# Kernel optimization log

Hardware: AMD Instinct MI355X
Metric: run time of the kernel (lower is better)

Reference implementation:

```python
import jax, jax.numpy as jnp
import numpy as np

C = 32        # channels per degree
NDEG = 4      # degrees 0..3
NLAYERS = 4   # hidden GSE3Res layers
OUTC = 64     # output fiber degree-0 channels
BATCH = 16
NPOINTS = 128
RBF_D = 16


def _sph(u):
    # real spherical harmonics l=0..3 on unit vectors u [E,3]
    x, y, z = u[:, 0], u[:, 1], u[:, 2]
    Y0 = 0.28209479177 * jnp.ones_like(x)[:, None]
    Y1 = 0.48860251190 * jnp.stack([y, z, x], -1)
    Y2 = jnp.stack([1.09254843059 * x * y, 1.09254843059 * y * z,
                    0.31539156525 * (3.0 * z * z - 1.0), 1.09254843059 * x * z,
                    0.54627421529 * (x * x - y * y)], -1)
    Y3 = jnp.stack([0.59004358992 * y * (3.0 * x * x - y * y), 2.89061144264 * x * y * z,
                    0.45704579946 * y * (5.0 * z * z - 1.0), 0.37317633259 * z * (5.0 * z * z - 3.0),
                    0.45704579946 * x * (5.0 * z * z - 1.0), 1.44530572132 * z * (x * x - y * y),
                    0.59004358992 * x * (x * x - 3.0 * y * y)], -1)
    return [Y0, Y1, Y2, Y3]


def _seg_softmax(logits, seg, n):
    m = jax.ops.segment_max(logits, seg, num_segments=n)
    e = jnp.exp(logits - m[seg])
    s = jax.ops.segment_sum(e, seg, num_segments=n)
    return e / s[seg]


def _forward(x, w1, b1, rW, sW, Wv, Wq, Wk, Wo, Wskip, gw, gb,
             w1o, b1o, roW, WvO, WqO, WkO, WoO, WskipO,
             Whid, bhid, Wout, bout, src, dst, gid):
    N = x.shape[0]
    rel = x[dst] - x[src]                                  # [E,3]
    d = jnp.sqrt((rel * rel).sum(-1) + 1e-12)              # [E]
    Ys = _sph(rel / d[:, None])
    centers = jnp.linspace(0.0, 4.0, RBF_D)
    rbf = jnp.exp(-((d[:, None] - centers) ** 2) / (2.0 * 0.5 ** 2))  # [E,16]
    # input fiber {1:1} is zeros_like(x) in the original -> start from zero features
    h = [jnp.zeros((N, C, 2 * l + 1), x.dtype) for l in range(NDEG)]
    for i in range(NLAYERS):
        rh = jax.nn.relu(rbf @ w1[i] + b1[i])              # [E,32] radial net
        q = h[0][:, :, 0] @ Wq[i]                          # [N,32] invariant query
        k = rh @ Wk[i]                                     # [E,32]
        logit = (q[dst] * k).sum(-1) / (C ** 0.5)
        alpha = _seg_softmax(logit, dst, N)
        h0s = h[0][src][:, :, 0]                           # [E,32]
        new = []
        for l in range(NDEG):
            hs = h[l][src]                                 # [E,C,2l+1]
            R = rh @ rW[i, l]                              # [E,C] same-degree radial gate
            S = rh @ sW[i, l]                              # [E,C] degree0->l path
            v = jnp.einsum('ecm,cd->edm', hs, Wv[i, l]) * R[:, :, None]
            v = v + (S * (h0s + 1.0))[:, :, None] * Ys[l][:, None, :]
            agg = jax.ops.segment_sum(alpha[:, None, None] * v, dst, num_segments=N)
            hn = (jnp.einsum('ncm,cd->ndm', h[l], Wskip[i, l])
                  + jnp.einsum('ncm,cd->ndm', agg, Wo[i, l]))
            # GNormBias: norm nonlinearity with learned scale/bias
            nrm = jnp.sqrt((hn * hn).sum(-1) + 1e-12)      # [N,C]
            phi = jax.nn.relu(nrm * gw[i, l] + gb[i, l])
            new.append(hn * (phi / (nrm + 1e-6))[:, :, None])
        h = new
    # final GSE3Res to degree-0 out fiber (64 channels)
    rh = jax.nn.relu(rbf @ w1o + b1o)
    q = h[0][:, :, 0] @ WqO                                # [N,64]
    k = rh @ WkO                                           # [E,64]
    logit = (q[dst] * k).sum(-1) / (OUTC ** 0.5)
    alpha = _seg_softmax(logit, dst, N)
    m0 = jnp.zeros((src.shape[0], OUTC), x.dtype)
    for l in range(NDEG):
        c = jnp.einsum('ecm,em->ec', h[l][src], Ys[l])     # invariant contraction
        m0 = m0 + (c @ WvO[l]) * (rh @ roW[l])
    agg = jax.ops.segment_sum(alpha[:, None] * m0, dst, num_segments=N)
    hout = agg @ WoO + h[0][:, :, 0] @ WskipO              # [N,64]
    # GAvgPooling per graph, then MLP head
    cnt = jax.ops.segment_sum(jnp.ones((N,), x.dtype), gid, num_segments=BATCH)
    pooled = jax.ops.segment_sum(hout, gid, num_segments=BATCH) / cnt[:, None]
    return jax.nn.relu(pooled @ Whid + bhid) @ Wout + bout  # [B,15]


def setup_inputs() -> dict:
    key = jax.random.key(0)
    ks = jax.random.split(key, 30)
    P, B = NPOINTS, BATCH
    N = B * P
    a = np.repeat(np.arange(P), P)
    b = np.tile(np.arange(P), P)
    m = a != b
    a, b = a[m], b[m]
    src = jnp.asarray(np.concatenate([a + g * P for g in range(B)]), jnp.int32)
    dst = jnp.asarray(np.concatenate([b + g * P for g in range(B)]), jnp.int32)
    gid = jnp.asarray(np.repeat(np.arange(B), P), jnp.int32)

    def w(k, shape, s=0.1):
        return (jax.random.normal(k, shape) * s).astype(jnp.float32)

    return {
        'x': jax.random.normal(ks[0], (N, 3), jnp.float32),
        'w1': w(ks[1], (4, 16, 32)), 'b1': w(ks[2], (4, 32)),
        'rW': w(ks[3], (4, 4, 32, 32)), 'sW': w(ks[4], (4, 4, 32, 32)),
        'Wv': w(ks[5], (4, 4, 32, 32)), 'Wq': w(ks[6], (4, 32, 32)), 'Wk': w(ks[7], (4, 32, 32)),
        'Wo': w(ks[8], (4, 4, 32, 32)), 'Wskip': w(ks[9], (4, 4, 32, 32)),
        'gw': w(ks[10], (4, 4, 32)), 'gb': w(ks[11], (4, 4, 32)) + 0.5,
        'w1o': w(ks[12], (16, 32)), 'b1o': w(ks[13], (32,)),
        'roW': w(ks[14], (4, 32, 64)), 'WvO': w(ks[15], (4, 32, 64)),
        'WqO': w(ks[16], (32, 64)), 'WkO': w(ks[17], (32, 64)),
        'WoO': w(ks[18], (64, 64)), 'WskipO': w(ks[19], (32, 64)),
        'Whid': w(ks[20], (64, 64)), 'bhid': w(ks[21], (64,)),
        'Wout': w(ks[22], (64, 15)), 'bout': w(ks[23], (15,)),
        'src': src, 'dst': dst, 'gid': gid,
    }


def reference(x, w1, b1, rW, sW, Wv, Wq, Wk, Wo, Wskip, gw, gb,
              w1o, b1o, roW, WvO, WqO, WkO, WoO, WskipO,
              Whid, bhid, Wout, bout, src, dst, gid):
    return _forward(x, w1, b1, rW, sW, Wv, Wq, Wk, Wo, Wskip, gw, gb,
                    w1o, b1o, roW, WvO, WqO, WkO, WoO, WskipO,
                    Whid, bhid, Wout, bout, src, dst, gid)
```

## Files before the change

kernel.cpp:

```cpp
#include <hip/hip_runtime.h>
#include <hip/hip_bf16.h>
#include <hip/hip_fp16.h>

#define NNODE 2048
#define NGRAPH 16

typedef _Float16 h2v __attribute__((ext_vector_type(2)));

__device__ __forceinline__ int lmap(int m) { return m == 0 ? 0 : (m < 4 ? 1 : (m < 9 ? 2 : 3)); }

__device__ __forceinline__ float f4get(const float4& v, int j) {
    return j == 0 ? v.x : (j == 1 ? v.y : (j == 2 ? v.z : v.w));
}
__device__ __forceinline__ uint32_t u4get(const uint4& v, int j) {
    return j == 0 ? v.x : (j == 1 ? v.y : (j == 2 ? v.z : v.w));
}

__device__ __forceinline__ uint32_t f2h2(float a, float b) {
    __half2 h2 = __floats2half2_rn(a, b);
    return *reinterpret_cast<uint32_t*>(&h2);
}
__device__ __forceinline__ float2 h2f2(uint32_t u) {
    __half2 h2 = *reinterpret_cast<__half2*>(&u);
    return __half22float2(h2);
}

__device__ __forceinline__ float fdot2u(uint32_t a, uint32_t b, float c) {
#if defined(__has_builtin)
#if __has_builtin(__builtin_amdgcn_fdot2)
    return __builtin_amdgcn_fdot2(__builtin_bit_cast(h2v, a), __builtin_bit_cast(h2v, b), c, false);
#else
    float2 af = h2f2(a), bf = h2f2(b);
    return fmaf(af.x, bf.x, fmaf(af.y, bf.y, c));
#endif
#else
    float2 af = h2f2(a), bf = h2f2(b);
    return fmaf(af.x, bf.x, fmaf(af.y, bf.y, c));
#endif
}

__device__ __forceinline__ void sph16(float x, float y, float z, float* Y) {
    Y[0] = 0.28209479177f;
    Y[1] = 0.4886025119f * y; Y[2] = 0.4886025119f * z; Y[3] = 0.4886025119f * x;
    Y[4] = 1.09254843059f * x * y;
    Y[5] = 1.09254843059f * y * z;
    Y[6] = 0.31539156525f * (3.f * z * z - 1.f);
    Y[7] = 1.09254843059f * x * z;
    Y[8] = 0.54627421529f * (x * x - y * y);
    Y[9]  = 0.59004358992f * y * (3.f * x * x - y * y);
    Y[10] = 2.89061144264f * x * y * z;
    Y[11] = 0.45704579946f * y * (5.f * z * z - 1.f);
    Y[12] = 0.37317633259f * z * (5.f * z * z - 3.f);
    Y[13] = 0.45704579946f * x * (5.f * z * z - 1.f);
    Y[14] = 1.44530572132f * z * (x * x - y * y);
    Y[15] = 0.59004358992f * x * (x * x - 3.f * y * y);
}

__device__ __constant__ float c_Cj[16] = {
    1.0f, 0.8674233f, 0.5661551f, 0.2780373f, 0.1027397f, 0.0285656f,
    5.97600e-3f, 9.40697e-4f, 1.11418e-4f, 9.92910e-6f, 6.65834e-7f,
    3.35950e-8f, 1.27541e-9f, 3.64326e-11f, 7.83070e-13f, 1.26642e-14f
};

#define PROC_SRC(aa, u0, u1, u2, u3, h0v) { \
    int a_ = a0 + (aa); \
    float w_ = alphas[a_]; \
    if (w_ != 0.f) { \
        const float4* yp = reinterpret_cast<const float4*>(&yss[a_ * 20]); \
        float4 y0 = yp[0], y1 = yp[1], y2 = yp[2], y3 = yp[3]; \
        float hb1 = (h0v) + 1.f; \
        float sc0 = S[aa][0] * hb1, sc1 = S[aa][1] * hb1; \
        float sc2 = S[aa][2] * hb1, sc3 = S[aa][3] * hb1; \
        acc[0]  = fmaf(w_, fmaf((u0).x, R[aa][0], sc0 * y0.x), acc[0]); \
        acc[1]  = fmaf(w_, fmaf((u0).y, R[aa][1], sc1 * y0.y), acc[1]); \
        acc[2]  = fmaf(w_, fmaf((u0).z, R[aa][1], sc1 * y0.z), acc[2]); \
        acc[3]  = fmaf(w_, fmaf((u0).w, R[aa][1], sc1 * y0.w), acc[3]); \
        acc[4]  = fmaf(w_, fmaf((u1).x, R[aa][2], sc2 * y1.x), acc[4]); \
        acc[5]  = fmaf(w_, fmaf((u1).y, R[aa][2], sc2 * y1.y), acc[5]); \
        acc[6]  = fmaf(w_, fmaf((u1).z, R[aa][2], sc2 * y1.z), acc[6]); \
        acc[7]  = fmaf(w_, fmaf((u1).w, R[aa][2], sc2 * y1.w), acc[7]); \
        acc[8]  = fmaf(w_, fmaf((u2).x, R[aa][2], sc2 * y2.x), acc[8]); \
        acc[9]  = fmaf(w_, fmaf((u2).y, R[aa][3], sc3 * y2.y), acc[9]); \
        acc[10] = fmaf(w_, fmaf((u2).z, R[aa][3], sc3 * y2.z), acc[10]); \
        acc[11] = fmaf(w_, fmaf((u2).w, R[aa][3], sc3 * y2.w), acc[11]); \
        acc[12] = fmaf(w_, fmaf((u3).x, R[aa][3], sc3 * y3.x), acc[12]); \
        acc[13] = fmaf(w_, fmaf((u3).y, R[aa][3], sc3 * y3.y), acc[13]); \
        acc[14] = fmaf(w_, fmaf((u3).z, R[aa][3], sc3 * y3.z), acc[14]); \
        acc[15] = fmaf(w_, fmaf((u3).w, R[aa][3], sc3 * y3.w), acc[15]); \
    } }

__global__ __launch_bounds__(256, 3) void k_layer(
    const float* __restrict__ x, const float* __restrict__ h,
    const float* __restrict__ h0in, const float* __restrict__ vpre,
    const float* __restrict__ wqk,
    const float* __restrict__ w1, const float* __restrict__ b1,
    const float* __restrict__ rW, const float* __restrict__ sW,
    const float* __restrict__ Wskip, const float* __restrict__ Wo,
    const float* __restrict__ gw, const float* __restrict__ gb,
    const float* __restrict__ Wv_n, const float* __restrict__ Wq_n, const float* __restrict__ Wk_n,
    const float* __restrict__ WvO, const float* __restrict__ WqO, const float* __restrict__ WkO,
    float* __restrict__ hnew, float* __restrict__ h0out,
    float* __restrict__ vpre_n, float* __restrict__ wqk_n,
    float* __restrict__ wq2, float* __restrict__ U,
    int layer, int last)
{
    __shared__ __align__(16) uint32_t rwswP[4096];
    __shared__ __align__(16) float rhs[128 * 36];
    __shared__ __align__(16) float yss[128 * 20];
    __shared__ __align__(16) float ub[1056];
    __shared__ __align__(16) float b1s[32];
    __shared__ __align__(16) float wqks[32];
    __shared__ float alphas[128];
    __shared__ float red[256];
    __shared__ float scale[128];
    __shared__ float sh_inv;

    int nblk = blockIdx.x, t = threadIdx.x;
    int g = nblk >> 7, b = nblk & 127;
    int gbase = g << 7;

    float* xs = ub;
    float* w1s = ub + 384;
    uint32_t* rh16 = reinterpret_cast<uint32_t*>(rhs);

    for (int o = t; o < 384; o += 256) xs[o] = x[gbase * 3 + o];
    for (int o = t; o < 512; o += 256) w1s[o] = w1[layer * 512 + o];
    if (t < 32) { b1s[t] = b1[layer * 32 + t]; wqks[t] = wqk[nblk * 32 + t]; }
    for (int idx = t; idx < 2048; idx += 256) {
        int d2 = idx & 31, j2 = (idx >> 5) & 15, l = idx >> 9;
        int src = layer * 4096 + l * 1024 + (2 * j2) * 32 + d2;
        int base = ((l * 16 + j2) << 6) + (d2 << 1);
        rwswP[base]     = f2h2(rW[src], rW[src + 32]);
        rwswP[base + 1] = f2h2(sW[src], sW[src + 32]);
    }
    __syncthreads();

    {
        int a = t & 127, dh = t >> 7;
        float rx = xs[b * 3 + 0] - xs[a * 3 + 0];
        float ry = xs[b * 3 + 1] - xs[a * 3 + 1];
        float rz = xs[b * 3 + 2] - xs[a * 3 + 2];
        float dd = sqrtf(rx * rx + ry * ry + rz * rz + 1e-12f);
        float inv = 1.f / dd;
        float ys[16];
        sph16(rx * inv, ry * inv, rz * inv, ys);
        if (dh == 0) {
#pragma unroll
            for (int m = 0; m < 16; m++) yss[a * 20 + m] = ys[m];
        }
        float rbf[16];
        {
            float e1 = __expf(1.06666666667f * dd);
            float mj = __expf(-2.f * dd * dd);
            rbf[0] = mj;
#pragma unroll
            for (int j = 1; j < 16; j++) { mj *= e1; rbf[j] = mj * c_Cj[j]; }
        }
        float4 sd0, sd1, sd2, sd3;
        {
            const float4* b4 = reinterpret_cast<const float4*>(&b1s[dh * 16]);
            sd0 = b4[0]; sd1 = b4[1]; sd2 = b4[2]; sd3 = b4[3];
        }
#pragma unroll
        for (int j = 0; j < 16; j++) {
            float rb = rbf[j];
            const float4* w4 = reinterpret_cast<const float4*>(&w1s[j * 32 + dh * 16]);
            float4 w0 = w4[0], wv1 = w4[1], wv2 = w4[2], wv3 = w4[3];
            sd0.x = fmaf(rb, w0.x, sd0.x);  sd0.y = fmaf(rb, w0.y, sd0.y);
            sd0.z = fmaf(rb, w0.z, sd0.z);  sd0.w = fmaf(rb, w0.w, sd0.w);
            sd1.x = fmaf(rb, wv1.x, sd1.x); sd1.y = fmaf(rb, wv1.y, sd1.y);
            sd1.z = fmaf(rb, wv1.z, sd1.z); sd1.w = fmaf(rb, wv1.w, sd1.w);
            sd2.x = fmaf(rb, wv2.x, sd2.x); sd2.y = fmaf(rb, wv2.y, sd2.y);
            sd2.z = fmaf(rb, wv2.z, sd2.z); sd2.w = fmaf(rb, wv2.w, sd2.w);
            sd3.x = fmaf(rb, wv3.x, sd3.x); sd3.y = fmaf(rb, wv3.y, sd3.y);
            sd3.z = fmaf(rb, wv3.z, sd3.z); sd3.w = fmaf(rb, wv3.w, sd3.w);
        }
        sd0.x = fmaxf(sd0.x, 0.f); sd0.y = fmaxf(sd0.y, 0.f);
        sd0.z = fmaxf(sd0.z, 0.f); sd0.w = fmaxf(sd0.w, 0.f);
        sd1.x = fmaxf(sd1.x, 0.f); sd1.y = fmaxf(sd1.y, 0.f);
        sd1.z = fmaxf(sd1.z, 0.f); sd1.w = fmaxf(sd1.w, 0.f);
        sd2.x = fmaxf(sd2.x, 0.f); sd2.y = fmaxf(sd2.y, 0.f);
        sd2.z = fmaxf(sd2.z, 0.f); sd2.w = fmaxf(sd2.w, 0.f);
        sd3.x = fmaxf(sd3.x, 0.f); sd3.y = fmaxf(sd3.y, 0.f);
        sd3.z = fmaxf(sd3.z, 0.f); sd3.w = fmaxf(sd3.w, 0.f);
        const float4* q4 = reinterpret_cast<const float4*>(&wqks[dh * 16]);
        float4 qa = q4[0], qb = q4[1], qc = q4[2], qd = q4[3];
        float lpart = 0.f;
        lpart = fmaf(sd0.x, qa.x, lpart); lpart = fmaf(sd0.y, qa.y, lpart);
        lpart = fmaf(sd0.z, qa.z, lpart); lpart = fmaf(sd0.w, qa.w, lpart);
        lpart = fmaf(sd1.x, qb.x, lpart); lpart = fmaf(sd1.y, qb.y, lpart);
        lpart = fmaf(sd1.z, qb.z, lpart); lpart = fmaf(sd1.w, qb.w, lpart);
        lpart = fmaf(sd2.x, qc.x, lpart); lpart = fmaf(sd2.y, qc.y, lpart);
        lpart = fmaf(sd2.z, qc.z, lpart); lpart = fmaf(sd2.w, qc.w, lpart);
        lpart = fmaf(sd3.x, qd.x, lpart); lpart = fmaf(sd3.y, qd.y, lpart);
        lpart = fmaf(sd3.z, qd.z, lpart); lpart = fmaf(sd3.w, qd.w, lpart);
        uint4 pk0, pk1;
        pk0.x = f2h2(sd0.x, sd0.y); pk0.y = f2h2(sd0.z, sd0.w);
        pk0.z = f2h2(sd1.x, sd1.y); pk0.w = f2h2(sd1.z, sd1.w);
        pk1.x = f2h2(sd2.x, sd2.y); pk1.y = f2h2(sd2.z, sd2.w);
        pk1.z = f2h2(sd3.x, sd3.y); pk1.w = f2h2(sd3.z, sd3.w);
        *reinterpret_cast<uint4*>(&rh16[a * 20 + dh * 8])     = pk0;
        *reinterpret_cast<uint4*>(&rh16[a * 20 + dh * 8 + 4]) = pk1;
        red[t] = lpart;
    }
    __syncthreads();
    if (t < 128) alphas[t] = (red[t] + red[t + 128]) * 0.17677669529663687f;
    __syncthreads();

    if (t < 128) {
        float m = (t != b) ? alphas[t] : -1e30f;
#pragma unroll
        for (int off = 32; off > 0; off >>= 1) m = fmaxf(m, __shfl_xor(m, off));
        if ((t & 63) == 0) red[t >> 6] = m;
    }
    __syncthreads();
    {
        float mx = fmaxf(red[0], red[1]);
        if (t < 128) {
            float e = (t != b) ? __expf(alphas[t] - mx) : 0.f;
            alphas[t] = e;
            float s = e;
#pragma unroll
            for (int off = 32; off > 0; off >>= 1) s += __shfl_xor(s, off);
            if ((t & 63) == 0) red[2 + (t >> 6)] = s;
        }
    }
    __syncthreads();
    if (t == 0) sh_inv = 1.f / (red[2] + red[3]);

    int grp = t >> 5, d = t & 31;
    float acc[16];
#pragma unroll
    for (int m = 0; m < 16; m++) acc[m] = 0.f;

    for (int chunk = 0; chunk < 2; chunk++) {
        int a0 = grp * 16 + chunk * 8;
        float R[8][4], S[8][4];
#pragma unroll
        for (int aa = 0; aa < 8; aa++)
#pragma unroll
            for (int l = 0; l < 4; l++) { R[aa][l] = 0.f; S[aa][l] = 0.f; }

#pragma unroll 2
        for (int j8 = 0; j8 < 4; j8++) {
            uint4 rq[8];
#pragma unroll
            for (int aa = 0; aa < 8; aa++)
                rq[aa] = *reinterpret_cast<const uint4*>(&rh16[(a0 + aa) * 20 + j8 * 4]);
#pragma unroll
            for (int l = 0; l < 4; l++) {
#pragma unroll
                for (int jp = 0; jp < 4; jp++) {
                    uint2 wp = *reinterpret_cast<const uint2*>(
                        &rwswP[((l * 16 + j8 * 4 + jp) << 6) + (d << 1)]);
#pragma unroll
                    for (int aa = 0; aa < 8; aa++) {
                        uint32_t rv = u4get(rq[aa], jp);
                        R[aa][l] = fdot2u(rv, wp.x, R[aa][l]);
                        S[aa][l] = fdot2u(rv, wp.y, S[aa][l]);
                    }
                }
            }
        }

        float4 A0, A1, A2, A3, B0, B1, B2, B3; float Ah, Bh;
        {
            const float4* p4 = reinterpret_cast<const float4*>(vpre + (gbase + a0) * 512 + d * 16);
            A0 = p4[0]; A1 = p4[1]; A2 = p4[2]; A3 = p4[3];
            Ah = h0in[(gbase + a0) * 32 + d];
            const float4* q4 = reinterpret_cast<const float4*>(vpre + (gbase + a0 + 1) * 512 + d * 16);
            B0 = q4[0]; B1 = q4[1]; B2 = q4[2]; B3 = q4[3];
            Bh = h0in[(gbase + a0 + 1) * 32 + d];
        }
#pragma unroll
        for (int ap = 0; ap < 4; ap++) {
            int aa = ap * 2;
            {
                float4 u0 = A0, u1 = A1, u2 = A2, u3 = A3; float h0v = Ah;
                if (ap < 3) {
                    const float4* p4 = reinterpret_cast<const float4*>(vpre + (gbase + a0 + aa + 2) * 512 + d * 16);
                    A0 = p4[0]; A1 = p4[1]; A2 = p4[2]; A3 = p4[3];
                    Ah = h0in[(gbase + a0 + aa + 2) * 32 + d];
                }
                PROC_SRC(aa, u0, u1, u2, u3, h0v)
            }
            {
                float4 u0 = B0, u1 = B1, u2 = B2, u3 = B3; float h0v = Bh;
                if (ap < 3) {
                    const float4* p4 = reinterpret_cast<const float4*>(vpre + (gbase + a0 + aa + 3) * 512 + d * 16);
                    B0 = p4[0]; B1 = p4[1]; B2 = p4[2]; B3 = p4[3];
                    Bh = h0in[(gbase + a0 + aa + 3) * 32 + d];
                }
                PROC_SRC(aa + 1, u0, u1, u2, u3, h0v)
            }
        }
    }
    __syncthreads();

    float* P = rhs;
#pragma unroll
    for (int m = 0; m < 16; m++) P[grp * 528 + m * 33 + d] = acc[m];
    float* hs = yss;
    for (int o = t; o < 512; o += 256) hs[o] = h[nblk * 512 + o];
    for (int o = t; o < 4096; o += 256) rwswP[o] = __float_as_uint(Wo[layer * 4096 + o]);
    __syncthreads();

    float* hnS = ub;
    float* aggL = ub + 528;
    float invs = sh_inv;
    for (int o = t; o < 512; o += 256) {
        int m = o >> 5, c = o & 31;
        float s = 0.f;
#pragma unroll
        for (int gg = 0; gg < 8; gg++) s += P[gg * 528 + m * 33 + c];
        aggL[m * 33 + c] = s * invs;
    }
    __syncthreads();

    for (int o = t; o < 4096; o += 256) rhs[o] = Wskip[layer * 4096 + o];
    __syncthreads();

    for (int o = t; o < 512; o += 256) {
        int m = o >> 5, dd = o & 31, l = lmap(m);
        float s = 0.f;
        const float* wa = &rhs[l * 1024 + dd];
        const uint32_t* wb = &rwswP[l * 1024 + dd];
        const float* hrow = &hs[m];
        const float* arow = &aggL[m * 33];
#pragma unroll
        for (int c = 0; c < 32; c++) {
            s = fmaf(hrow[c * 16], wa[c * 32], s);
            s = fmaf(arow[c], __uint_as_float(wb[c * 32]), s);
        }
        hnS[m * 33 + dd] = s;
    }
    __syncthreads();

    if (t < 128) {
        int dd = t >> 2, l = t & 3;
        int m0 = l * l, cnt = 2 * l + 1;
        float s = 1e-12f;
        for (int m = m0; m < m0 + cnt; m++) { float v = hnS[m * 33 + dd]; s = fmaf(v, v, s); }
        float nr = sqrtf(s);
        float phi = fmaxf(nr * gw[(layer * 4 + l) * 32 + dd] + gb[(layer * 4 + l) * 32 + dd], 0.f);
        scale[dd * 4 + l] = phi / (nr + 1e-6f);
    }
    if (!last) {
        for (int o = t; o < 4096; o += 256) rwswP[o] = __float_as_uint(Wv_n[o]);
    } else {
        for (int o = t; o < 4096; o += 256) {
            rhs[o] = WvO[o];
            rwswP[o] = __float_as_uint(WvO[4096 + o]);
        }
    }
    __syncthreads();

    for (int o = t; o < 512; o += 256) {
        int dd = o >> 4, m = o & 15;
        float v = hnS[m * 33 + dd] * scale[dd * 4 + lmap(m)];
        hnew[nblk * 512 + o] = v;
        hnS[m * 33 + dd] = v;
    }
    __syncthreads();

    if (t < 32) h0out[nblk * 32 + t] = hnS[t];

    if (!last) {
        for (int o = t; o < 512; o += 256) {
            int dd = o >> 4, m = o & 15, l = lmap(m);
            float s = 0.f;
            const uint32_t* wv = &rwswP[l * 1024 + dd];
            const float* hrow = &hnS[m * 33];
#pragma unroll
            for (int c = 0; c < 32; c++) s = fmaf(hrow[c], __uint_as_float(wv[c * 32]), s);
            vpre_n[nblk * 512 + o] = s;
        }
        if (t < 32) {
            float s = 0.f;
#pragma unroll
            for (int c = 0; c < 32; c++) s = fmaf(hnS[c * 33], Wq_n[c * 32 + t], s);
            red[t] = s;
        }
        __syncthreads();
        if (t < 32) {
            float s = 0.f;
#pragma unroll
            for (int j = 0; j < 32; j++) s = fmaf(Wk_n[t * 32 + j], red[j], s);
            wqk_n[nblk * 32 + t] = s;
        }
    } else {
        for (int o = t; o < 1024; o += 256) {
            int j = o >> 4, m = o & 15, l = lmap(m);
            float s = 0.f;
            const float* hrow = &hnS[m * 33];
            if (l < 2) {
                const float* wv = &rhs[l * 2048 + j];
#pragma unroll
                for (int c = 0; c < 32; c++) s = fmaf(hrow[c], wv[c * 64], s);
            } else {
                const uint32_t* wv = &rwswP[(l - 2) * 2048 + j];
#pragma unroll
                for (int c = 0; c < 32; c++) s = fmaf(hrow[c], __uint_as_float(wv[c * 64]), s);
            }
            U[nblk * 1024 + o] = s;
        }
        if (t < 64) {
            float s = 0.f;
#pragma unroll
            for (int c = 0; c < 32; c++) s = fmaf(hnS[c * 33], WqO[c * 64 + t], s);
            red[t] = s;
        }
        __syncthreads();
        if (t < 32) {
            float s = 0.f;
#pragma unroll
            for (int j = 0; j < 64; j++) s = fmaf(WkO[t * 64 + j], red[j], s);
            wq2[nblk * 32 + t] = s;
        }
    }
}

__global__ __launch_bounds__(256, 3) void k_out_edge(
    const float* __restrict__ x, const float* __restrict__ h0f,
    const float* __restrict__ w1o, const float* __restrict__ b1o,
    const float* __restrict__ wq2, const float* __restrict__ roW,
    const float* __restrict__ U, const float* __restrict__ WoO,
    const float* __restrict__ WskipO, float* __restrict__ hout)
{
    __shared__ uint32_t rosP[4096];
    __shared__ __align__(16) uint32_t rh16o[128 * 16];
    __shared__ __align__(16) float yss[128 * 20];
    __shared__ float xs[384];
    __shared__ float w1s[512];
    __shared__ float b1s[32];
    __shared__ float wq2s[32];
    __shared__ float alphas[128];
    __shared__ float red[256];
    __shared__ float agg64s[64];
    __shared__ float sh_inv;

    int n = blockIdx.x, t = threadIdx.x;
    int g = n >> 7, b = n & 127;
    int gbase = g << 7;

    for (int o = t; o < 384; o += 256) xs[o] = x[gbase * 3 + o];
    for (int o = t; o < 512; o += 256) w1s[o] = w1o[o];
    if (t < 32) { b1s[t] = b1o[t]; wq2s[t] = wq2[n * 32 + t]; }
    for (int o = t; o < 4096; o += 256) {
        int j = o & 63, lc = o >> 6, cp = lc & 15, l = lc >> 4;
        rosP[o] = f2h2(roW[(l * 32 + 2 * cp) * 64 + j], roW[(l * 32 + 2 * cp + 1) * 64 + j]);
    }
    __syncthreads();

    {
        int a = t & 127, dh = t >> 7;
        float rx = xs[b * 3 + 0] - xs[a * 3 + 0];
        float ry = xs[b * 3 + 1] - xs[a * 3 + 1];
        float rz = xs[b * 3 + 2] - xs[a * 3 + 2];
        float dd = sqrtf(rx * rx + ry * ry + rz * rz + 1e-12f);
        float inv = 1.f / dd;
        float ys[16];
        sph16(rx * inv, ry * inv, rz * inv, ys);
        if (dh == 0) {
#pragma unroll
            for (int m = 0; m < 16; m++) yss[a * 20 + m] = ys[m];
        }
        float rbf[16];
#pragma unroll
        for (int j = 0; j < 16; j++) {
            float dc = dd - (4.f / 15.f) * j;
            rbf[j] = __expf(-2.f * dc * dc);
        }
        float lpart = 0.f;
        int d0 = dh * 16;
        float sprev = 0.f;
        for (int d2 = 0; d2 < 16; d2++) {
            int d = d0 + d2;
            float s = b1s[d];
#pragma unroll
            for (int j = 0; j < 16; j++) s = fmaf(rbf[j], w1s[j * 32 + d], s);
            s = fmaxf(s, 0.f);
            lpart = fmaf(s, wq2s[d], lpart);
            if (d2 & 1) rh16o[a * 16 + dh * 8 + (d2 >> 1)] = f2h2(sprev, s);
            sprev = s;
        }
        red[t] = lpart;
    }
    __syncthreads();
    if (t < 128) alphas[t] = (red[t] + red[t + 128]) * 0.125f;
    __syncthreads();

    if (t < 128) {
        float m = (t != b) ? alphas[t] : -1e30f;
#pragma unroll
        for (int off = 32; off > 0; off >>= 1) m = fmaxf(m, __shfl_xor(m, off));
        if ((t & 63) == 0) red[t >> 6] = m;
    }
    __syncthreads();
    {
        float mx = fmaxf(red[0], red[1]);
        if (t < 128) {
            float e = (t != b) ? __expf(alphas[t] - mx) : 0.f;
            alphas[t] = e;
            float s = e;
#pragma unroll
            for (int off = 32; off > 0; off >>= 1) s += __shfl_xor(s, off);
            if ((t & 63) == 0) red[2 + (t >> 6)] = s;
        }
    }
    __syncthreads();
    if (t == 0) sh_inv = 1.f / (red[2] + red[3]);
    __syncthreads();

    int grp = t >> 6, j = t & 63;
    float accO = 0.f;
    for (int chunk = 0; chunk < 4; chunk++) {
        int a0 = grp * 32 + chunk * 8;
        float RO[8][4];
#pragma unroll
        for (int aa = 0; aa < 8; aa++)
#pragma unroll
            for (int l = 0; l < 4; l++) RO[aa][l] = 0.f;

#pragma unroll 2
        for (int q = 0; q < 4; q++) {
            uint4 rq[8];
#pragma unroll
            for (int aa = 0; aa < 8; aa++)
                rq[aa] = *reinterpret_cast<const uint4*>(&rh16o[(a0 + aa) * 16 + q * 4]);
#pragma unroll
            for (int l = 0; l < 4; l++) {
#pragma unroll
                for (int cp = 0; cp < 4; cp++) {
                    uint32_t wv = rosP[(l * 16 + q * 4 + cp) * 64 + j];
#pragma unroll
                    for (int aa = 0; aa < 8; aa++)
                        RO[aa][l] = fdot2u(u4get(rq[aa], cp), wv, RO[aa][l]);
                }
            }
        }

        float4 A0, A1, A2, A3, B0, B1, B2, B3;
        {
            const float4* p4 = reinterpret_cast<const float4*>(U + (gbase + a0) * 1024 + j * 16);
            A0 = p4[0]; A1 = p4[1]; A2 = p4[2]; A3 = p4[3];
            const float4* q4 = reinterpret_cast<const float4*>(U + (gbase + a0 + 1) * 1024 + j * 16);
            B0 = q4[0]; B1 = q4[1]; B2 = q4[2]; B3 = q4[3];
        }
#define PROC_O(aa, u0, u1, u2, u3) { \
        int a_ = a0 + (aa); \
        float w_ = alphas[a_]; \
        if (w_ != 0.f) { \
            const float4* yp = reinterpret_cast<const float4*>(&yss[a_ * 20]); \
            float4 y0 = yp[0], y1 = yp[1], y2 = yp[2], y3 = yp[3]; \
            float cv0 = y0.x * (u0).x; \
            float cv1 = fmaf(y0.y, (u0).y, fmaf(y0.z, (u0).z, y0.w * (u0).w)); \
            float cv2 = fmaf(y1.x, (u1).x, fmaf(y1.y, (u1).y, fmaf(y1.z, (u1).z, fmaf(y1.w, (u1).w, y2.x * (u2).x)))); \
            float cv3 = fmaf(y2.y, (u2).y, fmaf(y2.z, (u2).z, fmaf(y2.w, (u2).w, \
                        fmaf(y3.x, (u3).x, fmaf(y3.y, (u3).y, fmaf(y3.z, (u3).z, y3.w * (u3).w)))))); \
            float s_ = fmaf(cv0, RO[aa][0], fmaf(cv1, RO[aa][1], fmaf(cv2, RO[aa][2], cv3 * RO[aa][3]))); \
            accO = fmaf(w_, s_, accO); \
        } }
#pragma unroll
        for (int ap = 0; ap < 4; ap++) {
            int aa = ap * 2;
            {
                float4 u0 = A0, u1 = A1, u2 = A2, u3 = A3;
                if (ap < 3) {
                    const float4* p4 = reinterpret_cast<const float4*>(U + (gbase + a0 + aa + 2) * 1024 + j * 16);
                    A0 = p4[0]; A1 = p4[1]; A2 = p4[2]; A3 = p4[3];
                }
                PROC_O(aa, u0, u1, u2, u3)
            }
            {
                float4 u0 = B0, u1 = B1, u2 = B2, u3 = B3;
                if (ap < 3) {
                    const float4* p4 = reinterpret_cast<const float4*>(U + (gbase + a0 + aa + 3) * 1024 + j * 16);
                    B0 = p4[0]; B1 = p4[1]; B2 = p4[2]; B3 = p4[3];
                }
                PROC_O(aa + 1, u0, u1, u2, u3)
            }
        }
#undef PROC_O
    }
    red[t] = accO;
    __syncthreads();
    if (t < 64) agg64s[t] = (red[t] + red[64 + t] + red[128 + t] + red[192 + t]) * sh_inv;
    __syncthreads();

    if (t < 64) {
        float s = 0.f;
#pragma unroll
        for (int c = 0; c < 64; c++) s = fmaf(agg64s[c], WoO[c * 64 + t], s);
        const float* hr = &h0f[n * 32];
#pragma unroll
        for (int c = 0; c < 32; c++) s = fmaf(hr[c], WskipO[c * 64 + t], s);
        hout[n * 64 + t] = s;
    }
}

__global__ __launch_bounds__(64) void k_final(
    const float* __restrict__ hout, const float* __restrict__ Whid,
    const float* __restrict__ bhid, const float* __restrict__ Wout,
    const float* __restrict__ bout, float* __restrict__ out)
{
    __shared__ float pooled[64], hid[64];
    int g = blockIdx.x, t = threadIdx.x;
    float s = 0.f;
    for (int p = 0; p < 128; p++) s += hout[(g * 128 + p) * 64 + t];
    pooled[t] = s * (1.f / 128.f);
    __syncthreads();
    float hv = bhid[t];
#pragma unroll
    for (int c = 0; c < 64; c++) hv = fmaf(pooled[c], Whid[c * 64 + t], hv);
    hid[t] = fmaxf(hv, 0.f);
    __syncthreads();
    if (t < 15) {
        float o = bout[t];
#pragma unroll
        for (int c = 0; c < 64; c++) o = fmaf(hid[c], Wout[c * 15 + t], o);
        out[g * 15 + t] = o;
    }
}

extern "C" void kernel_launch(void* const* d_in, const int* in_sizes, int n_in,
                              void* d_out, int out_size, void* d_ws, size_t ws_size,
                              hipStream_t stream) {
    const float* x      = (const float*)d_in[0];
    const float* w1     = (const float*)d_in[1];
    const float* b1     = (const float*)d_in[2];
    const float* rW     = (const float*)d_in[3];
    const float* sW     = (const float*)d_in[4];
    const float* Wv     = (const float*)d_in[5];
    const float* Wq     = (const float*)d_in[6];
    const float* Wk     = (const float*)d_in[7];
    const float* Wo     = (const float*)d_in[8];
    const float* Wskip  = (const float*)d_in[9];
    const float* gw     = (const float*)d_in[10];
    const float* gb     = (const float*)d_in[11];
    const float* w1o    = (const float*)d_in[12];
    const float* b1o    = (const float*)d_in[13];
    const float* roW    = (const float*)d_in[14];
    const float* WvO    = (const float*)d_in[15];
    const float* WqO    = (const float*)d_in[16];
    const float* WkO    = (const float*)d_in[17];
    const float* WoO    = (const float*)d_in[18];
    const float* WskipO = (const float*)d_in[19];
    const float* Whid   = (const float*)d_in[20];
    const float* bhid   = (const float*)d_in[21];
    const float* Wout   = (const float*)d_in[22];
    const float* bout   = (const float*)d_in[23];
    float* out = (float*)d_out;

    float* ws = (float*)d_ws;
    float* h0    = ws;
    float* h1    = h0 + NNODE * 512;
    float* vA    = h1 + NNODE * 512;
    float* wqkA  = vA + NNODE * 512;
    float* vB    = wqkA + NNODE * 32;
    float* wqkB  = vB + NNODE * 512;
    float* wq2   = wqkB + NNODE * 32;
    float* U     = wq2 + NNODE * 32;
    float* hout  = U + NNODE * 1024;
    float* s0A   = hout + NNODE * 64;
    float* s0B   = s0A + NNODE * 32;

    hipMemsetAsync(h0, 0, NNODE * 512 * sizeof(float), stream);
    hipMemsetAsync(vA, 0, (NNODE * 512 + NNODE * 32) * sizeof(float), stream);
    hipMemsetAsync(s0A, 0, NNODE * 32 * sizeof(float), stream);

    for (int i = 0; i < 4; i++) {
        const float* hc  = (i & 1) ? h1 : h0;
        float*       hn  = (i & 1) ? h0 : h1;
        const float* vin  = (i & 1) ? vB : vA;
        const float* qin  = (i & 1) ? wqkB : wqkA;
        float*       vout = (i & 1) ? vA : vB;
        float*       qout = (i & 1) ? wqkA : wqkB;
        const float* s0in = (i & 1) ? s0B : s0A;
        float*       s0out= (i & 1) ? s0A : s0B;
        int last = (i == 3);
        k_layer<<<NNODE, 256, 0, stream>>>(
            x, hc, s0in, vin, qin, w1, b1, rW, sW, Wskip, Wo, gw, gb,
            Wv + (last ? 0 : (i + 1) * 4096),
            Wq + (last ? 0 : (i + 1) * 1024),
            Wk + (last ? 0 : (i + 1) * 1024),
            WvO, WqO, WkO,
            hn, s0out, vout, qout, wq2, U, i, last);
    }
    k_out_edge<<<NNODE, 256, 0, stream>>>(x, s0A, w1o, b1o, wq2, roW, U, WoO, WskipO, hout);
    k_final<<<NGRAPH, 64, 0, stream>>>(hout, Whid, bhid, Wout, bout, out);
}
```

Before: 511.6 us.

## Shrink k_layer LDS footprint to fit four blocks per CU

Cuts the shared-memory use of the layer kernel so launch bounds can go from 3 to 4 blocks per CU. It does this in four ways. The spherical-harmonic buffer now uses a dense stride of 16 with an XOR swizzle instead of padding. Partial accumulators are first reduced across wavefront halves with a shuffle, which halves the partial-sum buffer. Wskip and WvO are read straight from global memory instead of being staged in LDS. The reduction scratch arrays are merged into one. The price is more global/L2 traffic for the weight reads and extra shuffle work, in return for more resident blocks to hide latency.

```diff
diff --git a/kernel.cpp b/kernel.cpp
--- a/kernel.cpp
+++ b/kernel.cpp
@@ -66,8 +66,9 @@
     int a_ = a0 + (aa); \
     float w_ = alphas[a_]; \
     if (w_ != 0.f) { \
-        const float4* yp = reinterpret_cast<const float4*>(&yss[a_ * 20]); \
-        float4 y0 = yp[0], y1 = yp[1], y2 = yp[2], y3 = yp[3]; \
+        int sw_ = (a_ >> 4) & 3; \
+        const float4* yb = reinterpret_cast<const float4*>(&yss[a_ * 16]); \
+        float4 y0 = yb[0 ^ sw_], y1 = yb[1 ^ sw_], y2 = yb[2 ^ sw_], y3 = yb[3 ^ sw_]; \
         float hb1 = (h0v) + 1.f; \
         float sc0 = S[aa][0] * hb1, sc1 = S[aa][1] * hb1; \
         float sc2 = S[aa][2] * hb1, sc3 = S[aa][3] * hb1; \
@@ -89,7 +90,7 @@
         acc[15] = fmaf(w_, fmaf((u3).w, R[aa][3], sc3 * y3.w), acc[15]); \
     } }
 
-__global__ __launch_bounds__(256, 3) void k_layer(
+__global__ __launch_bounds__(256, 4) void k_layer(
     const float* __restrict__ x, const float* __restrict__ h,
     const float* __restrict__ h0in, const float* __restrict__ vpre,
     const float* __restrict__ wqk,
@@ -105,14 +106,13 @@
     int layer, int last)
 {
     __shared__ __align__(16) uint32_t rwswP[4096];
-    __shared__ __align__(16) float rhs[128 * 36];
-    __shared__ __align__(16) float yss[128 * 20];
-    __shared__ __align__(16) float ub[1056];
+    __shared__ __align__(16) float rhs[2640];
+    __shared__ __align__(16) float yss[2048];
+    __shared__ __align__(16) float ub[896];
     __shared__ __align__(16) float b1s[32];
     __shared__ __align__(16) float wqks[32];
     __shared__ float alphas[128];
-    __shared__ float red[256];
-    __shared__ float scale[128];
+    __shared__ float red128[128];
     __shared__ float sh_inv;
 
     int nblk = blockIdx.x, t = threadIdx.x;
@@ -145,8 +145,12 @@
         float ys[16];
         sph16(rx * inv, ry * inv, rz * inv, ys);
         if (dh == 0) {
-#pragma unroll
-            for (int m = 0; m < 16; m++) yss[a * 20 + m] = ys[m];
+            int sw = (a >> 4) & 3;
+            float4* yb = reinterpret_cast<float4*>(&yss[a * 16]);
+            yb[0 ^ sw] = make_float4(ys[0], ys[1], ys[2], ys[3]);
+            yb[1 ^ sw] = make_float4(ys[4], ys[5], ys[6], ys[7]);
+            yb[2 ^ sw] = make_float4(ys[8], ys[9], ys[10], ys[11]);
+            yb[3 ^ sw] = make_float4(ys[12], ys[13], ys[14], ys[15]);
         }
         float rbf[16];
         {
@@ -201,32 +205,32 @@
         pk1.z = f2h2(sd3.x, sd3.y); pk1.w = f2h2(sd3.z, sd3.w);
         *reinterpret_cast<uint4*>(&rh16[a * 20 + dh * 8])     = pk0;
         *reinterpret_cast<uint4*>(&rh16[a * 20 + dh * 8 + 4]) = pk1;
-        red[t] = lpart;
-    }
-    __syncthreads();
-    if (t < 128) alphas[t] = (red[t] + red[t + 128]) * 0.17677669529663687f;
+        if (dh == 1) red128[a] = lpart;
+        __syncthreads();
+        if (dh == 0) alphas[a] = (lpart + red128[a]) * 0.17677669529663687f;
+    }
     __syncthreads();
 
     if (t < 128) {
         float m = (t != b) ? alphas[t] : -1e30f;
 #pragma unroll
         for (int off = 32; off > 0; off >>= 1) m = fmaxf(m, __shfl_xor(m, off));
-        if ((t & 63) == 0) red[t >> 6] = m;
+        if ((t & 63) == 0) red128[t >> 6] = m;
     }
     __syncthreads();
     {
-        float mx = fmaxf(red[0], red[1]);
+        float mx = fmaxf(red128[0], red128[1]);
         if (t < 128) {
             float e = (t != b) ? __expf(alphas[t] - mx) : 0.f;
             alphas[t] = e;
             float s = e;
 #pragma unroll
             for (int off = 32; off > 0; off >>= 1) s += __shfl_xor(s, off);
-            if ((t & 63) == 0) red[2 + (t >> 6)] = s;
-        }
-    }
-    __syncthreads();
-    if (t == 0) sh_inv = 1.f / (red[2] + red[3]);
+            if ((t & 63) == 0) red128[2 + (t >> 6)] = s;
+        }
+    }
+    __syncthreads();
+    if (t == 0) sh_inv = 1.f / (red128[2] + red128[3]);
 
     int grp = t >> 5, d = t & 31;
     float acc[16];
@@ -295,47 +299,53 @@
             }
         }
     }
+#pragma unroll
+    for (int m = 0; m < 16; m++) acc[m] += __shfl_xor(acc[m], 32);
     __syncthreads();
 
     float* P = rhs;
-#pragma unroll
-    for (int m = 0; m < 16; m++) P[grp * 528 + m * 33 + d] = acc[m];
+    int w4i = t >> 6;
+    if ((t & 32) == 0) {
+#pragma unroll
+        for (int m = 0; m < 16; m++) P[w4i * 528 + m * 33 + d] = acc[m];
+    }
     float* hs = yss;
     for (int o = t; o < 512; o += 256) hs[o] = h[nblk * 512 + o];
     for (int o = t; o < 4096; o += 256) rwswP[o] = __float_as_uint(Wo[layer * 4096 + o]);
     __syncthreads();
 
     float* hnS = ub;
-    float* aggL = ub + 528;
+    float* aggL = rhs + 2112;
     float invs = sh_inv;
     for (int o = t; o < 512; o += 256) {
         int m = o >> 5, c = o & 31;
         float s = 0.f;
 #pragma unroll
-        for (int gg = 0; gg < 8; gg++) s += P[gg * 528 + m * 33 + c];
+        for (int ww = 0; ww < 4; ww++) s += P[ww * 528 + m * 33 + c];
         aggL[m * 33 + c] = s * invs;
     }
     __syncthreads();
 
-    for (int o = t; o < 4096; o += 256) rhs[o] = Wskip[layer * 4096 + o];
-    __syncthreads();
-
-    for (int o = t; o < 512; o += 256) {
-        int m = o >> 5, dd = o & 31, l = lmap(m);
-        float s = 0.f;
-        const float* wa = &rhs[l * 1024 + dd];
-        const uint32_t* wb = &rwswP[l * 1024 + dd];
-        const float* hrow = &hs[m];
-        const float* arow = &aggL[m * 33];
-#pragma unroll
-        for (int c = 0; c < 32; c++) {
-            s = fmaf(hrow[c * 16], wa[c * 32], s);
-            s = fmaf(arow[c], __uint_as_float(wb[c * 32]), s);
-        }
-        hnS[m * 33 + dd] = s;
-    }
-    __syncthreads();
-
+    {
+        const float* WskipL = Wskip + layer * 4096;
+        for (int o = t; o < 512; o += 256) {
+            int m = o >> 5, dd = o & 31, l = lmap(m);
+            float s = 0.f;
+            const float* wa = &WskipL[l * 1024 + dd];
+            const uint32_t* wb = &rwswP[l * 1024 + dd];
+            const float* hrow = &hs[m];
+            const float* arow = &aggL[m * 33];
+#pragma unroll
+            for (int c = 0; c < 32; c++) {
+                s = fmaf(hrow[c * 16], wa[c * 32], s);
+                s = fmaf(arow[c], __uint_as_float(wb[c * 32]), s);
+            }
+            hnS[m * 33 + dd] = s;
+        }
+    }
+    __syncthreads();
+
+    float* scale = red128;
     if (t < 128) {
         int dd = t >> 2, l = t & 3;
         int m0 = l * l, cnt = 2 * l + 1;
@@ -347,11 +357,6 @@
     }
     if (!last) {
         for (int o = t; o < 4096; o += 256) rwswP[o] = __float_as_uint(Wv_n[o]);
-    } else {
-        for (int o = t; o < 4096; o += 256) {
-            rhs[o] = WvO[o];
-            rwswP[o] = __float_as_uint(WvO[4096 + o]);
-        }
     }
     __syncthreads();
 
@@ -379,13 +384,13 @@
             float s = 0.f;
 #pragma unroll
             for (int c = 0; c < 32; c++) s = fmaf(hnS[c * 33], Wq_n[c * 32 + t], s);
-            red[t] = s;
+            red128[t] = s;
         }
         __syncthreads();
         if (t < 32) {
             float s = 0.f;
 #pragma unroll
-            for (int j = 0; j < 32; j++) s = fmaf(Wk_n[t * 32 + j], red[j], s);
+            for (int j = 0; j < 32; j++) s = fmaf(Wk_n[t * 32 + j], red128[j], s);
             wqk_n[nblk * 32 + t] = s;
         }
     } else {
@@ -393,28 +398,22 @@
             int j = o >> 4, m = o & 15, l = lmap(m);
             float s = 0.f;
             const float* hrow = &hnS[m * 33];
-            if (l < 2) {
-                const float* wv = &rhs[l * 2048 + j];
-#pragma unroll
-                for (int c = 0; c < 32; c++) s = fmaf(hrow[c], wv[c * 64], s);
-            } else {
-                const uint32_t* wv = &rwswP[(l - 2) * 2048 + j];
-#pragma unroll
-                for (int c = 0; c < 32; c++) s = fmaf(hrow[c], __uint_as_float(wv[c * 64]), s);
-            }
+            const float* wv = &WvO[l * 2048 + j];
+#pragma unroll
+            for (int c = 0; c < 32; c++) s = fmaf(hrow[c], wv[c * 64], s);
             U[nblk * 1024 + o] = s;
         }
         if (t < 64) {
             float s = 0.f;
 #pragma unroll
             for (int c = 0; c < 32; c++) s = fmaf(hnS[c * 33], WqO[c * 64 + t], s);
-            red[t] = s;
+            red128[t] = s;
         }
         __syncthreads();
         if (t < 32) {
             float s = 0.f;
 #pragma unroll
-            for (int j = 0; j < 64; j++) s = fmaf(WkO[t * 64 + j], red[j], s);
+            for (int j = 0; j < 64; j++) s = fmaf(WkO[t * 64 + j], red128[j], s);
             wq2[nblk * 32 + t] = s;
         }
     }
```

New measurement: 750.2 us. 46.6% more time.
